# Kernel tuning notes

Measured on AMD Instinct MI355X. Metric: run time of the kernel, lower is better.

The kernel has to match this reference:

```python
import jax, jax.numpy as jnp
import numpy as np

B = 32768      # batch size
D = 256        # embedding dim
C = 2048       # number of classes (label range)
WEIGHT = 1.0
TEMPERATURE = 0.3
EPS = 1e-12


def setup_inputs() -> dict:
    key = jax.random.key(0)
    k1, k2 = jax.random.split(key)
    features = jax.random.normal(k1, (B, D), dtype=jnp.float32)
    labels = jax.random.randint(k2, (B,), 0, C, dtype=jnp.int32)
    return {"features": features, "labels": labels, "epoch": 5}


def reference(features, labels, epoch):
    # L2-normalize embeddings (F.normalize, p=2, dim=1)
    norms = jnp.sqrt(jnp.sum(features * features, axis=1, keepdims=True))
    f = features / jnp.maximum(norms, EPS)                      # [B, D]

    # per-class segment sums / counts (vectorized replacement of the python loop)
    ones = jnp.ones((f.shape[0],), dtype=f.dtype)
    counts = jax.ops.segment_sum(ones, labels, num_segments=C)  # [C]
    sums = jax.ops.segment_sum(f, labels, num_segments=C)       # [C, D]
    centroids = sums / jnp.maximum(counts, 1.0)[:, None]        # [C, D] (mean; empty classes masked later)

    # leave-one-out positive centroid: (sum_class - f_i) / (n_class - 1)
    cnt_i = counts[labels]                                       # [B]
    c_p = (sums[labels] - f) / jnp.maximum(cnt_i - 1.0, 1.0)[:, None]
    d_p = jnp.sqrt(jnp.sum((f - c_p) ** 2, axis=1) + EPS)        # [B]

    # distances to all class centroids: ||f||=1 after normalization
    cn2 = jnp.sum(centroids * centroids, axis=1)                 # [C]
    d2 = 1.0 + cn2[None, :] - 2.0 * (f @ centroids.T)           # [B, C]
    d = jnp.sqrt(jnp.maximum(d2, EPS))

    # mask own class and empty (absent-in-batch) classes, take min negative distance
    class_ids = jnp.arange(C, dtype=labels.dtype)
    neg_mask = (counts[None, :] > 0) & (labels[:, None] != class_ids[None, :])
    d_n = jnp.min(jnp.where(neg_mask, d, jnp.inf), axis=1)       # [B]

    # samples are skipped if their class is a singleton or no negative class exists
    valid = (cnt_i > 1.0) & jnp.isfinite(d_n)
    d_n_safe = jnp.where(jnp.isfinite(d_n), d_n, 0.0)

    # temperature schedule: min(temperature + 0.02*epoch, 1)
    temp = min(TEMPERATURE + 0.02 * epoch, 1.0)

    # ln(1 + exp((d_p - d_n)/t)) == softplus
    loss_per_sample = jax.nn.softplus((d_p - d_n_safe) / temp)
    cnt = jnp.sum(valid.astype(f.dtype))
    loss = jnp.where(cnt > 0,
                     jnp.sum(jnp.where(valid, loss_per_sample, 0.0)) / jnp.maximum(cnt, 1.0),
                     0.0)
    return WEIGHT * loss
```

## Files before the change

### kernel.cpp

```cpp
#include <hip/hip_runtime.h>
#include <hip/hip_bf16.h>
#include <math.h>

constexpr int Bn = 32768;
constexpr int Dn = 256;
constexpr int Cn = 2048;
constexpr int NSPLIT = 4;
constexpr int CLS_PER_BLK = Cn / NSPLIT;
constexpr int TCLS = 32;
constexpr int NIT = CLS_PER_BLK / TCLS;
#define EPSF 1e-12f
#define INFF __builtin_inff()

typedef __bf16 bf16x8 __attribute__((ext_vector_type(8)));
typedef __bf16 bf16x4 __attribute__((ext_vector_type(4)));
typedef float  f32x4  __attribute__((ext_vector_type(4)));

__device__ inline void async_copy16(const void* g, void* l) {
    __builtin_amdgcn_global_load_lds(
        (const __attribute__((address_space(1))) void*)g,
        (__attribute__((address_space(3))) void*)l, 16, 0, 0);
}

__global__ __launch_bounds__(256) void k_prep(const float* __restrict__ feat,
                                              __bf16* __restrict__ fneg) {
    const int wave = threadIdx.x >> 6, lane = threadIdx.x & 63;
    const int s = blockIdx.x * 4 + wave;
    const float4 v = ((const float4*)(feat + (size_t)s * Dn))[lane];
    float ss = v.x * v.x + v.y * v.y + v.z * v.z + v.w * v.w;
    #pragma unroll
    for (int off = 1; off < 64; off <<= 1) ss += __shfl_xor(ss, off, 64);
    const float inv = -2.0f / fmaxf(sqrtf(ss), EPSF);
    bf16x4 bf;
    bf[0] = (__bf16)(v.x * inv); bf[1] = (__bf16)(v.y * inv);
    bf[2] = (__bf16)(v.z * inv); bf[3] = (__bf16)(v.w * inv);
    *(bf16x4*)(fneg + (size_t)s * Dn + lane * 4) = bf;
}

__global__ __launch_bounds__(1024) void k_sort(const int* __restrict__ labels,
                                               int* __restrict__ cnt_i,
                                               int* __restrict__ offs,
                                               int* __restrict__ order,
                                               float* __restrict__ accum,
                                               unsigned* __restrict__ donecnt) {
    __shared__ int sh_hist[Cn];
    __shared__ int part[1024];
    const int t = threadIdx.x;
    if (t < Cn / 2) { sh_hist[t * 2] = 0; sh_hist[t * 2 + 1] = 0; }
    if (t == 0) { accum[0] = 0.f; accum[1] = 0.f; *donecnt = 0u; }
    __syncthreads();
    const int4* lab4 = (const int4*)labels;
    #pragma unroll
    for (int i = t; i < Bn / 4; i += 1024) {
        const int4 l4 = lab4[i];
        atomicAdd(&sh_hist[l4.x], 1); atomicAdd(&sh_hist[l4.y], 1);
        atomicAdd(&sh_hist[l4.z], 1); atomicAdd(&sh_hist[l4.w], 1);
    }
    __syncthreads();
    const int h0 = sh_hist[t * 2], h1 = sh_hist[t * 2 + 1];
    const int sum = h0 + h1;
    int v = sum;
    part[t] = v; __syncthreads();
    for (int off = 1; off < 1024; off <<= 1) {
        int add = (t >= off) ? part[t - off] : 0;
        __syncthreads();
        v += add; part[t] = v;
        __syncthreads();
    }
    const int base = v - sum;
    cnt_i[t * 2] = h0;     cnt_i[t * 2 + 1] = h1;
    offs[t * 2] = base;    offs[t * 2 + 1] = base + h0;
    __syncthreads();
    sh_hist[t * 2] = base; sh_hist[t * 2 + 1] = base + h0;
    __syncthreads();
    #pragma unroll
    for (int i = t; i < Bn / 4; i += 1024) {
        const int4 l4 = lab4[i];
        const int s0 = i * 4;
        int pos;
        pos = atomicAdd(&sh_hist[l4.x], 1); order[pos] = s0;
        pos = atomicAdd(&sh_hist[l4.y], 1); order[pos] = s0 + 1;
        pos = atomicAdd(&sh_hist[l4.z], 1); order[pos] = s0 + 2;
        pos = atomicAdd(&sh_hist[l4.w], 1); order[pos] = s0 + 3;
    }
}

__global__ __launch_bounds__(256) void k_centseg(const __bf16* __restrict__ fneg,
                                                 const int* __restrict__ order,
                                                 const int* __restrict__ offs,
                                                 const int* __restrict__ cnt_i,
                                                 __bf16* __restrict__ centK,
                                                 float* __restrict__ cn2x) {
    const int wave = threadIdx.x >> 6, lane = threadIdx.x & 63;
    const int c = blockIdx.x * 4 + wave;
    const int n = cnt_i[c], start = offs[c];
    int myidx = 0;
    if (lane < n) myidx = order[start + lane];
    float sx = 0.f, sy = 0.f, sz = 0.f, sw = 0.f;
    const int nf = (n < 64) ? n : 64;
    for (int j = 0; j < nf; ++j) {
        const int idx = __shfl(myidx, j, 64);
        const bf16x4 v = *(const bf16x4*)(fneg + (size_t)idx * Dn + lane * 4);
        sx += -0.5f * (float)v[0]; sy += -0.5f * (float)v[1];
        sz += -0.5f * (float)v[2]; sw += -0.5f * (float)v[3];
    }
    for (int j = 64; j < n; ++j) {
        const int idx = order[start + j];
        const bf16x4 v = *(const bf16x4*)(fneg + (size_t)idx * Dn + lane * 4);
        sx += -0.5f * (float)v[0]; sy += -0.5f * (float)v[1];
        sz += -0.5f * (float)v[2]; sw += -0.5f * (float)v[3];
    }
    const float invn = 1.0f / fmaxf((float)n, 1.0f);
    const float cx = sx * invn, cy = sy * invn, cz = sz * invn, cw = sw * invn;
    bf16x4 cb; cb[0] = (__bf16)cx; cb[1] = (__bf16)cy; cb[2] = (__bf16)cz; cb[3] = (__bf16)cw;
    *(bf16x4*)(centK + ((size_t)(lane >> 1) * Cn + c) * 8 + (lane & 1) * 4) = cb;
    float ss = cx * cx + cy * cy + cz * cz + cw * cw;
    #pragma unroll
    for (int off = 1; off < 64; off <<= 1) ss += __shfl_xor(ss, off, 64);
    if (lane == 0) cn2x[c] = (n > 0) ? ss : INFF;
}

__global__ __launch_bounds__(256, 2) void k_main(const __bf16* __restrict__ fneg,
                                                 const int* __restrict__ labels,
                                                 const __bf16* __restrict__ centK,
                                                 const float* __restrict__ cn2x,
                                                 float* __restrict__ minval,
                                                 float* __restrict__ dotown) {
    __shared__ __align__(16) __bf16 sB[2][TCLS * Dn];
    __shared__ float s_cn2[CLS_PER_BLK];
    const int lane = threadIdx.x & 63, wave = threadIdx.x >> 6;
    const int m16 = lane & 15, quad = lane >> 4;
    const int sbase = blockIdx.x * 256 + wave * 64;
    const int c_begin = blockIdx.y * CLS_PER_BLK;

    bf16x8 a[4][8];
    #pragma unroll
    for (int p = 0; p < 4; ++p) {
        const __bf16* fr = fneg + (size_t)(sbase + p * 16 + m16) * Dn + quad * 8;
        #pragma unroll
        for (int t = 0; t < 8; ++t) a[p][t] = *(const bf16x8*)(fr + t * 32);
    }
    int lab[4][4];
    #pragma unroll
    for (int p = 0; p < 4; ++p)
        #pragma unroll
        for (int r = 0; r < 4; ++r)
            lab[p][r] = labels[sbase + p * 16 + quad * 4 + r];

    float rm[4][4], dacc[4][4];
    #pragma unroll
    for (int p = 0; p < 4; ++p)
        #pragma unroll
        for (int r = 0; r < 4; ++r) { rm[p][r] = INFF; dacc[p][r] = 0.0f; }

    auto stage = [&](int buf, int it) {
        const int c0 = c_begin + it * TCLS;
        #pragma unroll
        for (int j = 0; j < 4; ++j) {
            const int chunk = wave * 256 + j * 64 + lane;
            const int h  = chunk >> 9;
            const int kc = (chunk >> 4) & 31;
            const int n  = chunk & 15;
            const __bf16* g = centK + ((size_t)kc * Cn + (c0 + h * 16 + n)) * 8;
            __bf16* l = &sB[buf][(size_t)(wave * 256 + j * 64) * 8];
            async_copy16(g, l);
        }
    };

    stage(0, 0);
    for (int c = threadIdx.x; c < CLS_PER_BLK; c += 256) s_cn2[c] = cn2x[c_begin + c];
    __syncthreads();
    for (int it = 0; it < NIT; ++it) {
        const int cur = it & 1;
        if (it + 1 < NIT) stage(cur ^ 1, it + 1);
        #pragma unroll
        for (int hh = 0; hh < 2; ++hh) {
            const int ctile = it * TCLS + hh * 16;
            const float cn2v = s_cn2[ctile + m16];
            const __bf16* ls = &sB[cur][hh * 4096];
            f32x4 acc[4] = {{0.f,0.f,0.f,0.f},{0.f,0.f,0.f,0.f},
                            {0.f,0.f,0.f,0.f},{0.f,0.f,0.f,0.f}};
            #pragma unroll
            for (int t = 0; t < 8; ++t) {
                const bf16x8 b = *(const bf16x8*)(ls + t * 512 + lane * 8);
                #pragma unroll
                for (int p = 0; p < 4; ++p)
                    acc[p] = __builtin_amdgcn_mfma_f32_16x16x32_bf16(a[p][t], b, acc[p], 0, 0, 0);
            }
            const int crow = c_begin + ctile + m16;
            #pragma unroll
            for (int p = 0; p < 4; ++p)
                #pragma unroll
                for (int r = 0; r < 4; ++r) {
                    const bool own = (crow == lab[p][r]);
                    const float sel = own ? INFF : cn2v;
                    rm[p][r] = fminf(rm[p][r], sel + acc[p][r]);
                    dacc[p][r] += own ? acc[p][r] : 0.0f;
                }
        }
        __syncthreads();
    }
    #pragma unroll
    for (int off = 1; off < 16; off <<= 1)
        #pragma unroll
        for (int p = 0; p < 4; ++p)
            #pragma unroll
            for (int r = 0; r < 4; ++r) {
                rm[p][r] = fminf(rm[p][r], __shfl_xor(rm[p][r], off, 64));
                dacc[p][r] += __shfl_xor(dacc[p][r], off, 64);
            }
    if (m16 == 0) {
        float* mv = minval + (size_t)blockIdx.y * Bn;
        float* dv = dotown + (size_t)blockIdx.y * Bn;
        #pragma unroll
        for (int p = 0; p < 4; ++p)
            #pragma unroll
            for (int r = 0; r < 4; ++r) {
                mv[sbase + p * 16 + quad * 4 + r] = rm[p][r];
                dv[sbase + p * 16 + quad * 4 + r] = dacc[p][r];
            }
    }
}

__global__ __launch_bounds__(256) void k_final(const int* __restrict__ labels,
                                               const int* __restrict__ cnt_i,
                                               const float* __restrict__ cn2x,
                                               const float* __restrict__ minval,
                                               const float* __restrict__ dotown,
                                               const int* __restrict__ epoch,
                                               float* __restrict__ accum,
                                               unsigned* __restrict__ donecnt,
                                               float* __restrict__ out) {
    const int i = blockIdx.x * 256 + threadIdx.x;
    const int lane = threadIdx.x & 63;
    const float temp = fminf(0.3f + 0.02f * (float)(*epoch), 1.0f);
    float m = minval[i];
    float draw = dotown[i];
    #pragma unroll
    for (int k = 1; k < NSPLIT; ++k) {
        m = fminf(m, minval[(size_t)k * Bn + i]);
        draw += dotown[(size_t)k * Bn + i];
    }
    const int l = labels[i];
    const int n = cnt_i[l];
    const float nf = (float)n;
    const float cn2 = cn2x[l];
    const float fds = nf * (-0.5f * draw);
    const float fm1 = fmaxf(nf - 1.0f, 1.0f);
    const float fdcp = (fds - 1.0f) / fm1;
    const float cp2 = (nf * nf * cn2 - 2.0f * fds + 1.0f) / (fm1 * fm1);
    const float dp2 = 1.0f - 2.0f * fdcp + cp2;
    const float d_p = sqrtf(fmaxf(dp2, 0.0f) + EPSF);
    const bool finite = (m < 1e37f);
    const float d_n = finite ? sqrtf(fmaxf(1.0f + m, EPSF)) : 0.0f;
    const bool valid = (n > 1) && finite;
    const float x = (d_p - d_n) / temp;
    const float sp = fmaxf(x, 0.0f) + log1pf(expf(-fabsf(x)));
    float ws = valid ? sp : 0.0f, wc = valid ? 1.0f : 0.0f;
    #pragma unroll
    for (int off = 1; off < 64; off <<= 1) {
        ws += __shfl_xor(ws, off, 64);
        wc += __shfl_xor(wc, off, 64);
    }
    if (lane == 0) {
        atomicAdd(&accum[0], ws);
        atomicAdd(&accum[1], wc);
        __threadfence();
    }
    __syncthreads();
    if (threadIdx.x == 0) {
        const unsigned old = atomicAdd(donecnt, 1u);
        if (old == (unsigned)(gridDim.x - 1)) {
            __threadfence();
            const float s = __hip_atomic_load(&accum[0], __ATOMIC_RELAXED,
                                              __HIP_MEMORY_SCOPE_AGENT);
            const float c = __hip_atomic_load(&accum[1], __ATOMIC_RELAXED,
                                              __HIP_MEMORY_SCOPE_AGENT);
            out[0] = (c > 0.0f) ? (s / fmaxf(c, 1.0f)) : 0.0f;
        }
    }
}

extern "C" void kernel_launch(void* const* d_in, const int* in_sizes, int n_in,
                              void* d_out, int out_size, void* d_ws, size_t ws_size,
                              hipStream_t stream) {
    const float* feat  = (const float*)d_in[0];
    const int* labels  = (const int*)d_in[1];
    const int* epoch   = (const int*)d_in[2];
    float* out = (float*)d_out;
    char* ws = (char*)d_ws;

    size_t off = 0;
    __bf16* fneg     = (__bf16*)(ws + off); off += (size_t)Bn * Dn * 2;
    __bf16* centK    = (__bf16*)(ws + off); off += (size_t)Cn * Dn * 2;
    float*  cn2x     = (float*)(ws + off);  off += (size_t)Cn * 4;
    int*    cnt_i    = (int*)(ws + off);    off += (size_t)Cn * 4;
    int*    offs     = (int*)(ws + off);    off += (size_t)Cn * 4;
    int*    order    = (int*)(ws + off);    off += (size_t)Bn * 4;
    float*  minval   = (float*)(ws + off);  off += (size_t)NSPLIT * Bn * 4;
    float*  dotown   = (float*)(ws + off);  off += (size_t)NSPLIT * Bn * 4;
    float*  accum    = (float*)(ws + off);  off += 2 * 4;
    unsigned* donecnt = (unsigned*)(ws + off); off += 4;

    k_prep<<<Bn / 4, 256, 0, stream>>>(feat, fneg);
    k_sort<<<1, 1024, 0, stream>>>(labels, cnt_i, offs, order, accum, donecnt);
    k_centseg<<<Cn / 4, 256, 0, stream>>>(fneg, order, offs, cnt_i, centK, cn2x);
    dim3 g5(Bn / 256, NSPLIT);
    k_main<<<g5, 256, 0, stream>>>(fneg, labels, centK, cn2x, minval, dotown);
    k_final<<<Bn / 256, 256, 0, stream>>>(labels, cnt_i, cn2x, minval, dotown,
                                          epoch, accum, donecnt, out);
}
```

Baseline: 174.7 us.

## Split label sort into histogram/scan and parallel scatter; double class tile

Result: slower. 201.5 us (+15.3%).

```diff
diff --git a/kernel.cpp b/kernel.cpp
--- a/kernel.cpp
+++ b/kernel.cpp
@@ -7,7 +7,7 @@
 constexpr int Cn = 2048;
 constexpr int NSPLIT = 4;
 constexpr int CLS_PER_BLK = Cn / NSPLIT;
-constexpr int TCLS = 32;
+constexpr int TCLS = 64;
 constexpr int NIT = CLS_PER_BLK / TCLS;
 #define EPSF 1e-12f
 #define INFF __builtin_inff()
@@ -37,20 +37,19 @@
     *(bf16x4*)(fneg + (size_t)s * Dn + lane * 4) = bf;
 }
 
-__global__ __launch_bounds__(1024) void k_sort(const int* __restrict__ labels,
-                                               int* __restrict__ cnt_i,
-                                               int* __restrict__ offs,
-                                               int* __restrict__ order,
-                                               float* __restrict__ accum,
-                                               unsigned* __restrict__ donecnt) {
+__global__ __launch_bounds__(1024) void k_histscan(const int* __restrict__ labels,
+                                                   int* __restrict__ cnt_i,
+                                                   int* __restrict__ offs,
+                                                   int* __restrict__ offs_wk,
+                                                   float* __restrict__ accum,
+                                                   unsigned* __restrict__ donecnt) {
     __shared__ int sh_hist[Cn];
     __shared__ int part[1024];
     const int t = threadIdx.x;
-    if (t < Cn / 2) { sh_hist[t * 2] = 0; sh_hist[t * 2 + 1] = 0; }
+    sh_hist[t * 2] = 0; sh_hist[t * 2 + 1] = 0;
     if (t == 0) { accum[0] = 0.f; accum[1] = 0.f; *donecnt = 0u; }
     __syncthreads();
     const int4* lab4 = (const int4*)labels;
-    #pragma unroll
     for (int i = t; i < Bn / 4; i += 1024) {
         const int4 l4 = lab4[i];
         atomicAdd(&sh_hist[l4.x], 1); atomicAdd(&sh_hist[l4.y], 1);
@@ -68,21 +67,17 @@
         __syncthreads();
     }
     const int base = v - sum;
-    cnt_i[t * 2] = h0;     cnt_i[t * 2 + 1] = h1;
-    offs[t * 2] = base;    offs[t * 2 + 1] = base + h0;
-    __syncthreads();
-    sh_hist[t * 2] = base; sh_hist[t * 2 + 1] = base + h0;
-    __syncthreads();
-    #pragma unroll
-    for (int i = t; i < Bn / 4; i += 1024) {
-        const int4 l4 = lab4[i];
-        const int s0 = i * 4;
-        int pos;
-        pos = atomicAdd(&sh_hist[l4.x], 1); order[pos] = s0;
-        pos = atomicAdd(&sh_hist[l4.y], 1); order[pos] = s0 + 1;
-        pos = atomicAdd(&sh_hist[l4.z], 1); order[pos] = s0 + 2;
-        pos = atomicAdd(&sh_hist[l4.w], 1); order[pos] = s0 + 3;
-    }
+    cnt_i[t * 2]   = h0;        cnt_i[t * 2 + 1]   = h1;
+    offs[t * 2]    = base;      offs[t * 2 + 1]    = base + h0;
+    offs_wk[t * 2] = base;      offs_wk[t * 2 + 1] = base + h0;
+}
+
+__global__ __launch_bounds__(256) void k_scatter(const int* __restrict__ labels,
+                                                 int* __restrict__ offs_wk,
+                                                 int* __restrict__ order) {
+    const int i = blockIdx.x * 256 + threadIdx.x;
+    const int pos = atomicAdd(&offs_wk[labels[i]], 1);
+    order[pos] = i;
 }
 
 __global__ __launch_bounds__(256) void k_centseg(const __bf16* __restrict__ fneg,
@@ -156,13 +151,13 @@
     auto stage = [&](int buf, int it) {
         const int c0 = c_begin + it * TCLS;
         #pragma unroll
-        for (int j = 0; j < 4; ++j) {
-            const int chunk = wave * 256 + j * 64 + lane;
+        for (int j = 0; j < 8; ++j) {
+            const int chunk = wave * 512 + j * 64 + lane;
             const int h  = chunk >> 9;
             const int kc = (chunk >> 4) & 31;
             const int n  = chunk & 15;
             const __bf16* g = centK + ((size_t)kc * Cn + (c0 + h * 16 + n)) * 8;
-            __bf16* l = &sB[buf][(size_t)(wave * 256 + j * 64) * 8];
+            __bf16* l = &sB[buf][(size_t)(wave * 512 + j * 64) * 8];
             async_copy16(g, l);
         }
     };
@@ -174,7 +169,7 @@
         const int cur = it & 1;
         if (it + 1 < NIT) stage(cur ^ 1, it + 1);
         #pragma unroll
-        for (int hh = 0; hh < 2; ++hh) {
+        for (int hh = 0; hh < 4; ++hh) {
             const int ctile = it * TCLS + hh * 16;
             const float cn2v = s_cn2[ctile + m16];
             const __bf16* ls = &sB[cur][hh * 4096];
@@ -296,6 +291,7 @@
     float*  cn2x     = (float*)(ws + off);  off += (size_t)Cn * 4;
     int*    cnt_i    = (int*)(ws + off);    off += (size_t)Cn * 4;
     int*    offs     = (int*)(ws + off);    off += (size_t)Cn * 4;
+    int*    offs_wk  = (int*)(ws + off);    off += (size_t)Cn * 4;
     int*    order    = (int*)(ws + off);    off += (size_t)Bn * 4;
     float*  minval   = (float*)(ws + off);  off += (size_t)NSPLIT * Bn * 4;
     float*  dotown   = (float*)(ws + off);  off += (size_t)NSPLIT * Bn * 4;
@@ -303,7 +299,8 @@
     unsigned* donecnt = (unsigned*)(ws + off); off += 4;
 
     k_prep<<<Bn / 4, 256, 0, stream>>>(feat, fneg);
-    k_sort<<<1, 1024, 0, stream>>>(labels, cnt_i, offs, order, accum, donecnt);
+    k_histscan<<<1, 1024, 0, stream>>>(labels, cnt_i, offs, offs_wk, accum, donecnt);
+    k_scatter<<<Bn / 256, 256, 0, stream>>>(labels, offs_wk, order);
     k_centseg<<<Cn / 4, 256, 0, stream>>>(fneg, order, offs, cnt_i, centK, cn2x);
     dim3 g5(Bn / 256, NSPLIT);
     k_main<<<g5, 256, 0, stream>>>(fneg, labels, centK, cn2x, minval, dotown);
```
